# Kernel optimization log

Hardware: AMD Instinct MI355X
Metric: run time of the kernel (lower is better)

Reference implementation:

```python
import jax, jax.numpy as jnp
import numpy as np
from jax.ops import segment_sum, segment_max, segment_min

N_PER = 128        # nodes (pulses) per graph; graphs are contiguous blocks
NUM_GRAPHS = 2048  # must be a multiple of BATCH_SIZE
K = 4              # knn_graph k (from KNNAmp(4, ...))
BATCH_SIZE = 1024  # hardcoded in the torch module
L1, L2, L3, L4, L5, L6, L7 = 5, 64, 128, 94, 64, 32, 1
GRU_IN = 4 * L5    # 256
GRU_H = L6         # 32


def setup_inputs() -> dict:
    key = jax.random.key(0)
    ks = jax.random.split(key, 12)
    N = N_PER * NUM_GRAPHS
    s = 0.1
    return {
        "x": jax.random.normal(ks[0], (N, L1), jnp.float32),
        "batch": (jnp.arange(N) // N_PER).astype(jnp.int32),
        "h_1": jnp.zeros((2, BATCH_SIZE, GRU_H), jnp.float32),
        "W1": jax.random.normal(ks[1], (2 * L1, L2), jnp.float32) * s,
        "b1": jnp.zeros((L2,), jnp.float32),
        "W2": jax.random.normal(ks[2], (L2, L3), jnp.float32) * s,
        "b2": jnp.zeros((L3,), jnp.float32),
        "nn1_W": jax.random.normal(ks[3], (3 * L3, L4), jnp.float32) * s,
        "nn1_b": jnp.zeros((L4,), jnp.float32),
        "nn2_W": jax.random.normal(ks[4], (L4, L5), jnp.float32) * s,
        "nn2_b": jnp.zeros((L5,), jnp.float32),
        "nn4_W": jax.random.normal(ks[5], (GRU_H, L7), jnp.float32) * s,
        "nn4_b": jnp.zeros((L7,), jnp.float32),
        "wih0": jax.random.normal(ks[6], (3 * GRU_H, GRU_IN), jnp.float32) * s,
        "whh0": jax.random.normal(ks[7], (3 * GRU_H, GRU_H), jnp.float32) * s,
        "bih0": jnp.zeros((3 * GRU_H,), jnp.float32),
        "bhh0": jnp.zeros((3 * GRU_H,), jnp.float32),
        "wih1": jax.random.normal(ks[8], (3 * GRU_H, GRU_H), jnp.float32) * s,
        "whh1": jax.random.normal(ks[9], (3 * GRU_H, GRU_H), jnp.float32) * s,
        "bih1": jnp.zeros((3 * GRU_H,), jnp.float32),
        "bhh1": jnp.zeros((3 * GRU_H,), jnp.float32),
    }


def _knn_neighbors(pos):
    # pos: [N,3]; graphs are contiguous blocks of N_PER nodes -> per-graph KNN
    p = pos.reshape(NUM_GRAPHS, N_PER, 3)
    d2 = jnp.sum((p[:, :, None, :] - p[:, None, :, :]) ** 2, -1)  # [G,n,n]
    d2 = d2 + jnp.eye(N_PER, dtype=d2.dtype) * 1e10               # loop=False
    _, idx = jax.lax.top_k(-d2, K)                                 # [G,n,K]
    off = (jnp.arange(NUM_GRAPHS, dtype=idx.dtype) * N_PER)[:, None, None]
    return (idx + off).reshape(-1, K)  # [N,K] global source (neighbor) ids


def _gru_layer(seq_in, h0, wih, whh, bih, bhh):
    # PyTorch GRU cell math; gate order r, z, n.
    def step(h, xt):
        gi = xt @ wih.T + bih
        gh = h @ whh.T + bhh
        ir, iz, inn = jnp.split(gi, 3, -1)
        hr, hz, hn = jnp.split(gh, 3, -1)
        r = jax.nn.sigmoid(ir + hr)
        z = jax.nn.sigmoid(iz + hz)
        n = jnp.tanh(inn + r * hn)
        hnew = (1.0 - z) * n + z * h
        return hnew, hnew
    hT, ys = jax.lax.scan(step, h0, seq_in)
    return ys, hT


def reference(x, batch, h_1, W1, b1, W2, b2, nn1_W, nn1_b, nn2_W, nn2_b,
              nn4_W, nn4_b, wih0, whh0, bih0, bhh0, wih1, whh1, bih1, bhh1):
    N = x.shape[0]
    nbr = _knn_neighbors(x[:, :3])                       # int indices, non-diff
    x_i = jnp.broadcast_to(x[:, None, :], (N, K, L1))    # center features
    x_j = x[nbr]                                         # [N,K,5] gather
    feats = jnp.concatenate([x_i, x_j - x_i], -1)        # EdgeConv message input
    m = jax.nn.relu(jax.nn.relu(feats @ W1 + b1) @ W2 + b2)  # [N,K,128]
    # three EdgeConvs share the same MLP; compute messages once, aggregate 3 ways
    h = jax.nn.relu(jnp.concatenate([m.max(1), m.mean(1), m.sum(1)], 1))  # [N,384]
    h = jax.nn.relu(h @ nn1_W + nn1_b)
    h = h @ nn2_W + nn2_b                                # [N,64]
    a = segment_max(h, batch, num_segments=NUM_GRAPHS)
    bmin = segment_min(h, batch, num_segments=NUM_GRAPHS)
    c = segment_sum(h, batch, num_segments=NUM_GRAPHS)
    cnt = segment_sum(jnp.ones((N, 1), h.dtype), batch, num_segments=NUM_GRAPHS)
    d = c / cnt
    g = jax.nn.relu(jnp.concatenate([a, bmin, c, d], 1))  # [G,256]
    seq_len = NUM_GRAPHS // BATCH_SIZE
    # faithful to torch.reshape((seq, 256, 1024)).transpose(1,2)
    g = g.reshape(seq_len, GRU_IN, BATCH_SIZE).transpose(0, 2, 1)  # [T,B,256]
    out0, hT0 = _gru_layer(g, h_1[0], wih0, whh0, bih0, bhh0)
    out1, hT1 = _gru_layer(out0, h_1[1], wih1, whh1, bih1, bhh1)
    hT = jnp.stack([hT0, hT1], 0)                        # [2,B,32]
    # torch: reshape(x.transpose(1,2), (-1, 32))
    y = out1.transpose(0, 2, 1).reshape(-1, GRU_H)
    y = jax.nn.relu(y)
    y = jax.nn.relu(y @ nn4_W + nn4_b)                   # [T*B, 1]
    return y, hT
```

## Files before the change

### kernel.cpp

```cpp
#include <hip/hip_runtime.h>
#include <hip/hip_bf16.h>

#define NPER 128

__device__ __forceinline__ void ins4(float d, int id, float* bd, int* bi) {
    const bool c0 = d < bd[0], c1 = d < bd[1], c2 = d < bd[2], c3 = d < bd[3];
    bd[3] = c2 ? bd[2] : (c3 ? d : bd[3]);  bi[3] = c2 ? bi[2] : (c3 ? id : bi[3]);
    bd[2] = c1 ? bd[1] : (c2 ? d : bd[2]);  bi[2] = c1 ? bi[1] : (c2 ? id : bi[2]);
    bd[1] = c0 ? bd[0] : (c1 ? d : bd[1]);  bi[1] = c0 ? bi[0] : (c1 ? id : bi[1]);
    bd[0] = c0 ? d : bd[0];                 bi[0] = c0 ? id : bi[0];
}

__global__ void k_prep(const float* __restrict__ W2,
                       const float* __restrict__ nn2W,
                       const float* __restrict__ nn1W,
                       float* __restrict__ W2I, float* __restrict__ nn2WT,
                       float* __restrict__ WfT)
{
    int i = blockIdx.x * 256 + threadIdx.x;
    if (i < 8192) {
        int ch4 = i >> 8, rem = i & 255, c = rem >> 2, sub = rem & 3;
        W2I[i] = W2[c * 128 + (ch4 * 4 + sub)];
    } else if (i < 8192 + 6016) {
        int j = i - 8192, ch = j / 94, c = j - ch * 94;
        nn2WT[j] = nn2W[c * 64 + ch];
    } else if (i < 8192 + 6016 + 24576) {
        int k = i - 14208, jj = k >> 8, r = k & 255;
        float v = 0.0f;
        if (jj < 94) {
            if (r < 128) v = nn1W[r * 94 + jj];
            else {
                int c = r - 128;
                v = 0.25f * nn1W[(128 + c) * 94 + jj] + nn1W[(256 + c) * 94 + jj];
            }
        }
        WfT[k] = v;
    }
}

__global__ __launch_bounds__(256, 2) void k_edge(
    const float* __restrict__ x,
    const float* __restrict__ W1,
    const float* __restrict__ b1,
    const float* __restrict__ W2I,
    const float* __restrict__ b2,
    const float* __restrict__ WfT,
    const float* __restrict__ nn1b,
    const float* __restrict__ nn2WT,
    const float* __restrict__ nn2b,
    float* __restrict__ pmax,
    float* __restrict__ pmin,
    float* __restrict__ psum)
{
    __shared__ float pool[10240];
    float* XS  = pool;
    float* KD  = pool + 640;
    int*   KI  = (int*)(pool + 1664);
    int*   NBR = (int*)(pool + 2688);
    float* AGM = pool;
    float* AGS = pool + 4352;
    float* NNH = pool;
    float* HT  = pool + 6016;

    const int t = threadIdx.x;
    const int lane = t & 63;
    const int w = __builtin_amdgcn_readfirstlane(t >> 6);
    const int graph = blockIdx.x >> 1;
    const int node0 = (blockIdx.x & 1) * 64;

    for (int i = t; i < NPER * 5; i += 256) XS[i] = x[(size_t)graph * (NPER * 5) + i];
    __syncthreads();

    {
        const int nl2 = t & 63;
        const int q  = t >> 6;
        const int ng2 = node0 + nl2;
        const float px = XS[ng2 * 5 + 0], py = XS[ng2 * 5 + 1], pz = XS[ng2 * 5 + 2];
        float bd[4] = {3e38f, 3e38f, 3e38f, 3e38f};
        int   bi[4] = {0, 0, 0, 0};
        const int m0 = q * 32;
        for (int m = m0; m < m0 + 32; ++m) {
            float dx = XS[m * 5 + 0] - px, dy = XS[m * 5 + 1] - py, dz = XS[m * 5 + 2] - pz;
            float d2 = __fadd_rn(__fadd_rn(__fmul_rn(dx, dx), __fmul_rn(dy, dy)),
                                 __fmul_rn(dz, dz));
            d2 = (m == ng2) ? 3.0e38f : d2;
            ins4(d2, m, bd, bi);
        }
        #pragma unroll
        for (int s = 0; s < 4; ++s) { KD[(q * 4 + s) * 64 + nl2] = bd[s]; KI[(q * 4 + s) * 64 + nl2] = bi[s]; }
    }
    __syncthreads();
    if (t < 64) {
        float bd[4] = {3e38f, 3e38f, 3e38f, 3e38f};
        int   bi[4] = {0, 0, 0, 0};
        #pragma unroll
        for (int q = 0; q < 4; ++q)
            #pragma unroll
            for (int s = 0; s < 4; ++s)
                ins4(KD[(q * 4 + s) * 64 + t], KI[(q * 4 + s) * 64 + t], bd, bi);
        #pragma unroll
        for (int s = 0; s < 4; ++s) NBR[t * 4 + s] = bi[s];
    }
    __syncthreads();

    const int nl = t >> 2;
    const int kk = t & 3;
    const int n_g = node0 + nl;
    const int j   = NBR[nl * 4 + kk];
    float f[10];
    #pragma unroll
    for (int d = 0; d < 5; ++d) { f[d] = XS[n_g * 5 + d]; f[5 + d] = XS[j * 5 + d] - f[d]; }
    float h1v[64];
    #pragma unroll
    for (int c = 0; c < 64; ++c) h1v[c] = b1[c];
    #pragma unroll
    for (int d = 0; d < 10; ++d) {
        float fd = f[d];
        #pragma unroll
        for (int c = 0; c < 64; ++c) h1v[c] = fmaf(fd, W1[d * 64 + c], h1v[c]);
    }
    #pragma unroll
    for (int c = 0; c < 64; ++c) h1v[c] = fmaxf(h1v[c], 0.0f);
    __syncthreads();

    float acc[24];
    const int jj0 = __builtin_amdgcn_readfirstlane(w * 24);
    #pragma unroll
    for (int i = 0; i < 24; ++i) acc[i] = (jj0 + i < 94) ? nn1b[jj0 + i] : 0.0f;

    for (int h = 0; h < 2; ++h) {
        for (int ch = 0; ch < 64; ch += 4) {
            const float* wp = W2I + (size_t)(h * 16 + (ch >> 2)) * 256;
            float m0 = b2[h * 64 + ch], m1 = b2[h * 64 + ch + 1];
            float m2 = b2[h * 64 + ch + 2], m3 = b2[h * 64 + ch + 3];
            #pragma unroll
            for (int c = 0; c < 64; ++c) {
                float hv = h1v[c];
                m0 = fmaf(hv, wp[c * 4 + 0], m0);
                m1 = fmaf(hv, wp[c * 4 + 1], m1);
                m2 = fmaf(hv, wp[c * 4 + 2], m2);
                m3 = fmaf(hv, wp[c * 4 + 3], m3);
            }
            m0 = fmaxf(m0, 0.0f); m1 = fmaxf(m1, 0.0f);
            m2 = fmaxf(m2, 0.0f); m3 = fmaxf(m3, 0.0f);
            float x0 = fmaxf(m0, __shfl_xor(m0, 1));
            float x1 = fmaxf(m1, __shfl_xor(m1, 1));
            float x2 = fmaxf(m2, __shfl_xor(m2, 1));
            float x3 = fmaxf(m3, __shfl_xor(m3, 1));
            x0 = fmaxf(x0, __shfl_xor(x0, 2));
            x1 = fmaxf(x1, __shfl_xor(x1, 2));
            x2 = fmaxf(x2, __shfl_xor(x2, 2));
            x3 = fmaxf(x3, __shfl_xor(x3, 2));
            float s0 = m0 + __shfl_xor(m0, 1);
            float s1 = m1 + __shfl_xor(m1, 1);
            float s2 = m2 + __shfl_xor(m2, 1);
            float s3 = m3 + __shfl_xor(m3, 1);
            s0 += __shfl_xor(s0, 2);
            s1 += __shfl_xor(s1, 2);
            s2 += __shfl_xor(s2, 2);
            s3 += __shfl_xor(s3, 2);
            if (kk == 0) {
                *(float4*)&AGM[nl * 68 + ch] = make_float4(x0, x1, x2, x3);
                *(float4*)&AGS[nl * 68 + ch] = make_float4(s0, s1, s2, s3);
            }
        }
        __syncthreads();

        for (int cb = 0; cb < 64; cb += 8) {
            float am[8], as_[8];
            #pragma unroll
            for (int i = 0; i < 2; ++i) {
                *(float4*)&am[i * 4]  = *(const float4*)&AGM[lane * 68 + cb + i * 4];
                *(float4*)&as_[i * 4] = *(const float4*)&AGS[lane * 68 + cb + i * 4];
            }
            #pragma unroll
            for (int i2 = 0; i2 < 24; ++i2) {
                const float* wa = WfT + (size_t)(jj0 + i2) * 256 + h * 64 + cb;
                const float* wb = wa + 128;
                float a = acc[i2];
                #pragma unroll
                for (int i = 0; i < 8; ++i) a = fmaf(am[i], wa[i], fmaf(as_[i], wb[i], a));
                acc[i2] = a;
            }
        }
        __syncthreads();
    }

    #pragma unroll
    for (int i2 = 0; i2 < 24; ++i2)
        if (jj0 + i2 < 94) NNH[(jj0 + i2) * 64 + lane] = fmaxf(acc[i2], 0.0f);
    __syncthreads();

    {
        const int ch0 = __builtin_amdgcn_readfirstlane(w * 16);
        float acc2[16];
        #pragma unroll
        for (int i = 0; i < 16; ++i) acc2[i] = nn2b[ch0 + i];
        #pragma unroll 1
        for (int cb = 0; cb < 64; cb += 32) {
            float hv[32];
            #pragma unroll
            for (int i = 0; i < 32; ++i) hv[i] = NNH[(cb + i) * 64 + lane];
            #pragma unroll
            for (int i = 0; i < 16; ++i) {
                const float* wp = nn2WT + (size_t)(ch0 + i) * 94 + cb;
                float a = acc2[i];
                #pragma unroll
                for (int c = 0; c < 32; ++c) a = fmaf(hv[c], wp[c], a);
                acc2[i] = a;
            }
        }
        {
            float hv[30];
            #pragma unroll
            for (int i = 0; i < 30; ++i) hv[i] = NNH[(64 + i) * 64 + lane];
            #pragma unroll
            for (int i = 0; i < 16; ++i) {
                const float* wp = nn2WT + (size_t)(ch0 + i) * 94 + 64;
                float a = acc2[i];
                #pragma unroll
                for (int c = 0; c < 30; ++c) a = fmaf(hv[c], wp[c], a);
                acc2[i] = a;
            }
        }
        #pragma unroll
        for (int i = 0; i < 8; ++i)
            *(float2*)&HT[lane * 66 + ch0 + i * 2] =
                make_float2(acc2[i * 2], acc2[i * 2 + 1]);
    }
    __syncthreads();

    if (t < 64) {
        float mx = -3e38f, mn = 3e38f, sm = 0.0f;
        for (int n = 0; n < 64; ++n) {
            float v = HT[n * 66 + t];
            mx = fmaxf(mx, v); mn = fminf(mn, v); sm += v;
        }
        pmax[(size_t)blockIdx.x * 64 + t] = mx;
        pmin[(size_t)blockIdx.x * 64 + t] = mn;
        psum[(size_t)blockIdx.x * 64 + t] = sm;
    }
}

__global__ void k_pool(const float* __restrict__ pmax, const float* __restrict__ pmin,
                       const float* __restrict__ psum, float* __restrict__ g_out)
{
    const int t = threadIdx.x;
    const int g = blockIdx.x * 4 + (t >> 6);
    const int ch = t & 63;
    const size_t a = (size_t)(2 * g) * 64 + ch, b = a + 64;
    float mx = fmaxf(pmax[a], pmax[b]);
    float mn = fminf(pmin[a], pmin[b]);
    float sm = psum[a] + psum[b];
    float* gp = g_out + (size_t)g * 256;
    gp[ch]        = fmaxf(mx, 0.0f);
    gp[64 + ch]   = fmaxf(mn, 0.0f);
    gp[128 + ch]  = fmaxf(sm, 0.0f);
    gp[192 + ch]  = fmaxf(sm * (1.0f / 128.0f), 0.0f);
}

__global__ __launch_bounds__(128) void k_gru(
    const float* __restrict__ g, const float* __restrict__ h1_in,
    const float* __restrict__ wih0, const float* __restrict__ whh0,
    const float* __restrict__ bih0, const float* __restrict__ bhh0,
    const float* __restrict__ wih1, const float* __restrict__ whh1,
    const float* __restrict__ bih1, const float* __restrict__ bhh1,
    float* __restrict__ out1, float* __restrict__ hT)
{
    __shared__ float xt[4][256];
    __shared__ float h0[4][32];
    __shared__ float h1l[4][32];
    const int tid = threadIdx.x;
    const int e = tid >> 5;
    const int j = tid & 31;
    const int b = blockIdx.x * 4 + e;

    h0[e][j]  = h1_in[b * 32 + j];
    h1l[e][j] = h1_in[32768 + b * 32 + j];
    __syncthreads();

    for (int t = 0; t < 2; ++t) {
        for (int c = j; c < 256; c += 32)
            xt[e][c] = g[(size_t)(t * 1024 + 4 * c + (b >> 8)) * 256 + (b & 255)];
        __syncthreads();

        float gi0 = bih0[j], gi1 = bih0[32 + j], gi2 = bih0[64 + j];
        for (int c = 0; c < 256; ++c) {
            float xv = xt[e][c];
            gi0 += xv * wih0[j * 256 + c];
            gi1 += xv * wih0[(32 + j) * 256 + c];
            gi2 += xv * wih0[(64 + j) * 256 + c];
        }
        float gh0 = bhh0[j], gh1 = bhh0[32 + j], gh2 = bhh0[64 + j];
        #pragma unroll
        for (int c = 0; c < 32; ++c) {
            float hv = h0[e][c];
            gh0 += hv * whh0[j * 32 + c];
            gh1 += hv * whh0[(32 + j) * 32 + c];
            gh2 += hv * whh0[(64 + j) * 32 + c];
        }
        float r = 1.0f / (1.0f + expf(-(gi0 + gh0)));
        float z = 1.0f / (1.0f + expf(-(gi1 + gh1)));
        float nn = tanhf(gi2 + r * gh2);
        float hn0 = (1.0f - z) * nn + z * h0[e][j];
        __syncthreads();
        h0[e][j] = hn0;
        __syncthreads();

        float ai0 = bih1[j], ai1 = bih1[32 + j], ai2 = bih1[64 + j];
        #pragma unroll
        for (int c = 0; c < 32; ++c) {
            float xv = h0[e][c];
            ai0 += xv * wih1[j * 32 + c];
            ai1 += xv * wih1[(32 + j) * 32 + c];
            ai2 += xv * wih1[(64 + j) * 32 + c];
        }
        float ah0 = bhh1[j], ah1 = bhh1[32 + j], ah2 = bhh1[64 + j];
        #pragma unroll
        for (int c = 0; c < 32; ++c) {
            float hv = h1l[e][c];
            ah0 += hv * whh1[j * 32 + c];
            ah1 += hv * whh1[(32 + j) * 32 + c];
            ah2 += hv * whh1[(64 + j) * 32 + c];
        }
        float r1 = 1.0f / (1.0f + expf(-(ai0 + ah0)));
        float z1 = 1.0f / (1.0f + expf(-(ai1 + ah1)));
        float n1 = tanhf(ai2 + r1 * ah2);
        float hn1 = (1.0f - z1) * n1 + z1 * h1l[e][j];
        __syncthreads();
        h1l[e][j] = hn1;
        out1[(size_t)(t * 1024 + b) * 32 + j] = hn1;
        __syncthreads();
    }
    hT[b * 32 + j]         = h0[e][j];
    hT[32768 + b * 32 + j] = h1l[e][j];
}

__global__ void k_final(const float* __restrict__ out1,
                        const float* __restrict__ nn4W, const float* __restrict__ nn4b,
                        float* __restrict__ y)
{
    const int r = blockIdx.x * 256 + threadIdx.x;
    if (r >= 2048) return;
    const int t = r >> 10, rp = r & 1023;
    const int f = rp >> 5, bb0 = (rp & 31) << 5;
    float acc = nn4b[0];
    #pragma unroll
    for (int c = 0; c < 32; ++c)
        acc += fmaxf(out1[(size_t)(t * 1024 + bb0 + c) * 32 + f], 0.0f) * nn4W[c];
    y[r] = fmaxf(acc, 0.0f);
}

extern "C" void kernel_launch(void* const* d_in, const int* in_sizes, int n_in,
                              void* d_out, int out_size, void* d_ws, size_t ws_size,
                              hipStream_t stream) {
    const float* x    = (const float*)d_in[0];
    const float* h1i  = (const float*)d_in[2];
    const float* W1   = (const float*)d_in[3];
    const float* b1   = (const float*)d_in[4];
    const float* W2   = (const float*)d_in[5];
    const float* b2   = (const float*)d_in[6];
    const float* nn1W = (const float*)d_in[7];
    const float* nn1b = (const float*)d_in[8];
    const float* nn2W = (const float*)d_in[9];
    const float* nn2b = (const float*)d_in[10];
    const float* nn4W = (const float*)d_in[11];
    const float* nn4b = (const float*)d_in[12];
    const float* wih0 = (const float*)d_in[13];
    const float* whh0 = (const float*)d_in[14];
    const float* bih0 = (const float*)d_in[15];
    const float* bhh0 = (const float*)d_in[16];
    const float* wih1 = (const float*)d_in[17];
    const float* whh1 = (const float*)d_in[18];
    const float* bih1 = (const float*)d_in[19];
    const float* bhh1 = (const float*)d_in[20];

    float* ws = (float*)d_ws;
    float* g_buf  = ws;
    float* out1   = g_buf + 524288;
    float* W2I    = out1 + 65536;
    float* nn2WT  = W2I + 8192;
    float* WfT    = nn2WT + 6016;
    float* pmax   = WfT + 24576;
    float* pmin   = pmax + 262144;
    float* psum   = pmin + 262144;

    float* y  = (float*)d_out;
    float* hT = y + 2048;

    hipLaunchKernelGGL(k_prep, dim3(152), dim3(256), 0, stream,
                       W2, nn2W, nn1W, W2I, nn2WT, WfT);
    hipLaunchKernelGGL(k_edge, dim3(4096), dim3(256), 0, stream,
                       x, W1, b1, W2I, b2, WfT, nn1b, nn2WT, nn2b,
                       pmax, pmin, psum);
    hipLaunchKernelGGL(k_pool, dim3(512), dim3(256), 0, stream,
                       pmax, pmin, psum, g_buf);
    hipLaunchKernelGGL(k_gru, dim3(256), dim3(128), 0, stream,
                       g_buf, h1i, wih0, whh0, bih0, bhh0,
                       wih1, whh1, bih1, bhh1, out1, hT);
    hipLaunchKernelGGL(k_final, dim3(8), dim3(256), 0, stream,
                       out1, nn4W, nn4b, y);
}
```

Measured before the change: 894.3 us.

## Process whole graph per block and fuse pooling into edge kernel; widen W2 tiles

Each k_edge block now loops over both 64-node halves of a graph and does the per-graph max/min/sum/mean pooling itself. This removes the k_pool launch and the partial-result buffers in global memory. The W2 weight interleave is widened from 4 to 8 output channels per pass, giving more independent FMAs per loaded h1 value. In exchange the grid is halved to 2048 blocks, which lowers parallelism, and the 8-wide accumulators raise register pressure.

```diff
diff --git a/kernel.cpp b/kernel.cpp
--- a/kernel.cpp
+++ b/kernel.cpp
@@ -14,13 +14,13 @@
 __global__ void k_prep(const float* __restrict__ W2,
                        const float* __restrict__ nn2W,
                        const float* __restrict__ nn1W,
-                       float* __restrict__ W2I, float* __restrict__ nn2WT,
+                       float* __restrict__ W2I8, float* __restrict__ nn2WT,
                        float* __restrict__ WfT)
 {
     int i = blockIdx.x * 256 + threadIdx.x;
     if (i < 8192) {
-        int ch4 = i >> 8, rem = i & 255, c = rem >> 2, sub = rem & 3;
-        W2I[i] = W2[c * 128 + (ch4 * 4 + sub)];
+        int ch8 = i >> 9, rem = i & 511, c = rem >> 3, sub = rem & 7;
+        W2I8[i] = W2[c * 128 + (ch8 * 8 + sub)];
     } else if (i < 8192 + 6016) {
         int j = i - 8192, ch = j / 94, c = j - ch * 94;
         nn2WT[j] = nn2W[c * 64 + ch];
@@ -42,15 +42,13 @@
     const float* __restrict__ x,
     const float* __restrict__ W1,
     const float* __restrict__ b1,
-    const float* __restrict__ W2I,
+    const float* __restrict__ W2I8,
     const float* __restrict__ b2,
     const float* __restrict__ WfT,
     const float* __restrict__ nn1b,
     const float* __restrict__ nn2WT,
     const float* __restrict__ nn2b,
-    float* __restrict__ pmax,
-    float* __restrict__ pmin,
-    float* __restrict__ psum)
+    float* __restrict__ g_out)
 {
     __shared__ float pool[10240];
     float* XS  = pool;
@@ -65,8 +63,12 @@
     const int t = threadIdx.x;
     const int lane = t & 63;
     const int w = __builtin_amdgcn_readfirstlane(t >> 6);
-    const int graph = blockIdx.x >> 1;
-    const int node0 = (blockIdx.x & 1) * 64;
+    const int graph = blockIdx.x;
+
+    float gmx = -3.0e38f, gmn = 3.0e38f, gsm = 0.0f;
+
+    #pragma unroll 1
+    for (int node0 = 0; node0 < 128; node0 += 64) {
 
     for (int i = t; i < NPER * 5; i += 256) XS[i] = x[(size_t)graph * (NPER * 5) + i];
     __syncthreads();
@@ -129,39 +131,65 @@
     for (int i = 0; i < 24; ++i) acc[i] = (jj0 + i < 94) ? nn1b[jj0 + i] : 0.0f;
 
     for (int h = 0; h < 2; ++h) {
-        for (int ch = 0; ch < 64; ch += 4) {
-            const float* wp = W2I + (size_t)(h * 16 + (ch >> 2)) * 256;
-            float m0 = b2[h * 64 + ch], m1 = b2[h * 64 + ch + 1];
+        for (int ch = 0; ch < 64; ch += 8) {
+            const float* wp = W2I8 + (size_t)(h * 8 + (ch >> 3)) * 512;
+            float m0 = b2[h * 64 + ch + 0], m1 = b2[h * 64 + ch + 1];
             float m2 = b2[h * 64 + ch + 2], m3 = b2[h * 64 + ch + 3];
+            float m4 = b2[h * 64 + ch + 4], m5 = b2[h * 64 + ch + 5];
+            float m6 = b2[h * 64 + ch + 6], m7 = b2[h * 64 + ch + 7];
             #pragma unroll
             for (int c = 0; c < 64; ++c) {
                 float hv = h1v[c];
-                m0 = fmaf(hv, wp[c * 4 + 0], m0);
-                m1 = fmaf(hv, wp[c * 4 + 1], m1);
-                m2 = fmaf(hv, wp[c * 4 + 2], m2);
-                m3 = fmaf(hv, wp[c * 4 + 3], m3);
+                m0 = fmaf(hv, wp[c * 8 + 0], m0);
+                m1 = fmaf(hv, wp[c * 8 + 1], m1);
+                m2 = fmaf(hv, wp[c * 8 + 2], m2);
+                m3 = fmaf(hv, wp[c * 8 + 3], m3);
+                m4 = fmaf(hv, wp[c * 8 + 4], m4);
+                m5 = fmaf(hv, wp[c * 8 + 5], m5);
+                m6 = fmaf(hv, wp[c * 8 + 6], m6);
+                m7 = fmaf(hv, wp[c * 8 + 7], m7);
             }
             m0 = fmaxf(m0, 0.0f); m1 = fmaxf(m1, 0.0f);
             m2 = fmaxf(m2, 0.0f); m3 = fmaxf(m3, 0.0f);
+            m4 = fmaxf(m4, 0.0f); m5 = fmaxf(m5, 0.0f);
+            m6 = fmaxf(m6, 0.0f); m7 = fmaxf(m7, 0.0f);
             float x0 = fmaxf(m0, __shfl_xor(m0, 1));
             float x1 = fmaxf(m1, __shfl_xor(m1, 1));
             float x2 = fmaxf(m2, __shfl_xor(m2, 1));
             float x3 = fmaxf(m3, __shfl_xor(m3, 1));
+            float x4 = fmaxf(m4, __shfl_xor(m4, 1));
+            float x5 = fmaxf(m5, __shfl_xor(m5, 1));
+            float x6 = fmaxf(m6, __shfl_xor(m6, 1));
+            float x7 = fmaxf(m7, __shfl_xor(m7, 1));
             x0 = fmaxf(x0, __shfl_xor(x0, 2));
             x1 = fmaxf(x1, __shfl_xor(x1, 2));
             x2 = fmaxf(x2, __shfl_xor(x2, 2));
             x3 = fmaxf(x3, __shfl_xor(x3, 2));
+            x4 = fmaxf(x4, __shfl_xor(x4, 2));
+            x5 = fmaxf(x5, __shfl_xor(x5, 2));
+            x6 = fmaxf(x6, __shfl_xor(x6, 2));
+            x7 = fmaxf(x7, __shfl_xor(x7, 2));
             float s0 = m0 + __shfl_xor(m0, 1);
             float s1 = m1 + __shfl_xor(m1, 1);
             float s2 = m2 + __shfl_xor(m2, 1);
             float s3 = m3 + __shfl_xor(m3, 1);
+            float s4 = m4 + __shfl_xor(m4, 1);
+            float s5 = m5 + __shfl_xor(m5, 1);
+            float s6 = m6 + __shfl_xor(m6, 1);
+            float s7 = m7 + __shfl_xor(m7, 1);
             s0 += __shfl_xor(s0, 2);
             s1 += __shfl_xor(s1, 2);
             s2 += __shfl_xor(s2, 2);
             s3 += __shfl_xor(s3, 2);
+            s4 += __shfl_xor(s4, 2);
+            s5 += __shfl_xor(s5, 2);
+            s6 += __shfl_xor(s6, 2);
+            s7 += __shfl_xor(s7, 2);
             if (kk == 0) {
-                *(float4*)&AGM[nl * 68 + ch] = make_float4(x0, x1, x2, x3);
-                *(float4*)&AGS[nl * 68 + ch] = make_float4(s0, s1, s2, s3);
+                *(float4*)&AGM[nl * 68 + ch]     = make_float4(x0, x1, x2, x3);
+                *(float4*)&AGM[nl * 68 + ch + 4] = make_float4(x4, x5, x6, x7);
+                *(float4*)&AGS[nl * 68 + ch]     = make_float4(s0, s1, s2, s3);
+                *(float4*)&AGS[nl * 68 + ch + 4] = make_float4(s4, s5, s6, s7);
             }
         }
         __syncthreads();
@@ -231,32 +259,23 @@
     __syncthreads();
 
     if (t < 64) {
-        float mx = -3e38f, mn = 3e38f, sm = 0.0f;
+        float mx2 = -3.0e38f, mn2 = 3.0e38f, sm2 = 0.0f;
         for (int n = 0; n < 64; ++n) {
             float v = HT[n * 66 + t];
-            mx = fmaxf(mx, v); mn = fminf(mn, v); sm += v;
-        }
-        pmax[(size_t)blockIdx.x * 64 + t] = mx;
-        pmin[(size_t)blockIdx.x * 64 + t] = mn;
-        psum[(size_t)blockIdx.x * 64 + t] = sm;
-    }
-}
-
-__global__ void k_pool(const float* __restrict__ pmax, const float* __restrict__ pmin,
-                       const float* __restrict__ psum, float* __restrict__ g_out)
-{
-    const int t = threadIdx.x;
-    const int g = blockIdx.x * 4 + (t >> 6);
-    const int ch = t & 63;
-    const size_t a = (size_t)(2 * g) * 64 + ch, b = a + 64;
-    float mx = fmaxf(pmax[a], pmax[b]);
-    float mn = fminf(pmin[a], pmin[b]);
-    float sm = psum[a] + psum[b];
-    float* gp = g_out + (size_t)g * 256;
-    gp[ch]        = fmaxf(mx, 0.0f);
-    gp[64 + ch]   = fmaxf(mn, 0.0f);
-    gp[128 + ch]  = fmaxf(sm, 0.0f);
-    gp[192 + ch]  = fmaxf(sm * (1.0f / 128.0f), 0.0f);
+            mx2 = fmaxf(mx2, v); mn2 = fminf(mn2, v); sm2 += v;
+        }
+        gmx = fmaxf(gmx, mx2); gmn = fminf(gmn, mn2); gsm += sm2;
+    }
+
+    }
+
+    if (t < 64) {
+        float* gp = g_out + (size_t)graph * 256;
+        gp[t]        = fmaxf(gmx, 0.0f);
+        gp[64 + t]   = fmaxf(gmn, 0.0f);
+        gp[128 + t]  = fmaxf(gsm, 0.0f);
+        gp[192 + t]  = fmaxf(gsm * (1.0f / 128.0f), 0.0f);
+    }
 }
 
 __global__ __launch_bounds__(128) void k_gru(
@@ -378,23 +397,17 @@
     float* ws = (float*)d_ws;
     float* g_buf  = ws;
     float* out1   = g_buf + 524288;
-    float* W2I    = out1 + 65536;
-    float* nn2WT  = W2I + 8192;
+    float* W2I8   = out1 + 65536;
+    float* nn2WT  = W2I8 + 8192;
     float* WfT    = nn2WT + 6016;
-    float* pmax   = WfT + 24576;
-    float* pmin   = pmax + 262144;
-    float* psum   = pmin + 262144;
 
     float* y  = (float*)d_out;
     float* hT = y + 2048;
 
     hipLaunchKernelGGL(k_prep, dim3(152), dim3(256), 0, stream,
-                       W2, nn2W, nn1W, W2I, nn2WT, WfT);
-    hipLaunchKernelGGL(k_edge, dim3(4096), dim3(256), 0, stream,
-                       x, W1, b1, W2I, b2, WfT, nn1b, nn2WT, nn2b,
-                       pmax, pmin, psum);
-    hipLaunchKernelGGL(k_pool, dim3(512), dim3(256), 0, stream,
-                       pmax, pmin, psum, g_buf);
+                       W2, nn2W, nn1W, W2I8, nn2WT, WfT);
+    hipLaunchKernelGGL(k_edge, dim3(2048), dim3(256), 0, stream,
+                       x, W1, b1, W2I8, b2, WfT, nn1b, nn2WT, nn2b, g_buf);
     hipLaunchKernelGGL(k_gru, dim3(256), dim3(128), 0, stream,
                        g_buf, h1i, wih0, whh0, bih0, bhh0,
                        wih1, whh1, bih1, bhh1, out1, hT);
```

Result: slower. 1.215 ms (+35.9%).
